# Kernel optimization log

Hardware: AMD Instinct MI355X
Metric: run time of the kernel (lower is better)

Reference implementation:

```python
import jax, jax.numpy as jnp
import numpy as np

D = 256; NH = 8; NL = 4; NP = 8; DFF = 1024; NQ = 300; BS = 8
DH = D // NH
_SHAPES = np.array([[100, 100], [50, 50], [25, 25], [13, 13]], dtype=np.int64)
S = int(_SHAPES.prod(1).sum())


def setup_inputs():
    key = jax.random.key(0)
    ks = jax.random.split(key, 24)
    rn = lambda k, sh, s=0.02: jax.random.normal(k, sh, jnp.float32) * s
    lsi = np.concatenate([[0], np.cumsum(_SHAPES.prod(1))[:-1]])
    return {
        'tgt': rn(ks[0], (NQ, BS, D), 1.0),
        'tgt_query_mask': rn(ks[1], (NQ, BS, D), 1.0),
        'tgt_reference_bboxs': jax.random.uniform(ks[2], (NQ, BS, 4), jnp.float32, 0.1, 0.5),
        'tgt_reference_masks': jax.random.uniform(ks[3], (NQ, BS, 32, 32), jnp.float32),
        'memory': rn(ks[4], (S, BS, D), 1.0),
        'in_proj_w': rn(ks[5], (3 * D, D)), 'in_proj_b': jnp.zeros((3 * D,), jnp.float32),
        'out_sa_w': rn(ks[6], (D, D)), 'out_sa_b': jnp.zeros((D,), jnp.float32),
        'norm2_g': jnp.ones((D,), jnp.float32), 'norm2_b': jnp.zeros((D,), jnp.float32),
        'value_w': rn(ks[7], (D, D)), 'value_b': jnp.zeros((D,), jnp.float32),
        'off_w': rn(ks[8], (NH * NL * NP * 2, D)), 'off_b': rn(ks[9], (NH * NL * NP * 2,), 0.5),
        'aw_w': rn(ks[10], (NH * NL * NP, D)), 'aw_b': jnp.zeros((NH * NL * NP,), jnp.float32),
        'out_ca_w': rn(ks[11], (D, D)), 'out_ca_b': jnp.zeros((D,), jnp.float32),
        'norm1_g': jnp.ones((D,), jnp.float32), 'norm1_b': jnp.zeros((D,), jnp.float32),
        'lin1_w': rn(ks[12], (DFF, D)), 'lin1_b': jnp.zeros((DFF,), jnp.float32),
        'lin2_w': rn(ks[13], (D, DFF)), 'lin2_b': jnp.zeros((D,), jnp.float32),
        'norm3_g': jnp.ones((D,), jnp.float32), 'norm3_b': jnp.zeros((D,), jnp.float32),
        'memory_key_padding_mask': jnp.zeros((BS, S), bool),
        'memory_spatial_shapes': jnp.asarray(_SHAPES, jnp.int32),
        'memory_level_start_index': jnp.asarray(lsi, jnp.int32),
    }


def _lin(x, w, b):
    return x @ w.T + b


def _ln(x, g, b):
    mu = x.mean(-1, keepdims=True)
    v = ((x - mu) ** 2).mean(-1, keepdims=True)
    return (x - mu) / jnp.sqrt(v + 1e-5) * g + b


def _ms_deform(query, ref, mem, pad_mask, spatial, lstart, vw, vb, ow, ob, aww, awb, outw, outb):
    # query/ref/mem: (bs, nq, D), (bs, nq, 4 cxcywh in [0,1]), (bs, S, D)
    bs, nq, _ = query.shape
    value = _lin(mem, vw, vb)
    value = jnp.where(pad_mask[:, :, None], 0.0, value).reshape(bs, -1, NH, DH)
    off = _lin(query, ow, ob).reshape(bs, nq, NH, NL, NP, 2)
    aw = jax.nn.softmax(_lin(query, aww, awb).reshape(bs, nq, NH, NL * NP), -1)
    aw = aw.reshape(bs, nq, NH, NL, NP)
    ref6 = ref[:, :, None, None, None, :]
    loc = ref6[..., :2] + off / NP * ref6[..., 2:4] * 0.5  # (bs,nq,NH,NL,NP,2)
    Hs = spatial[:, 0].reshape(1, 1, 1, NL, 1)
    Ws = spatial[:, 1].reshape(1, 1, 1, NL, 1)
    ls = lstart.reshape(1, 1, 1, NL, 1)
    Hf = Hs.astype(jnp.float32); Wf = Ws.astype(jnp.float32)
    # grid_sample align_corners=False pixel coords
    x = loc[..., 0] * Wf - 0.5
    y = loc[..., 1] * Hf - 0.5
    x0 = jnp.floor(x); y0 = jnp.floor(y)
    vT = value.transpose(2, 0, 1, 3)  # (NH,bs,S,DH)
    acc = jnp.zeros((bs, nq, NH, NL, NP, DH), jnp.float32)
    for dx in (0.0, 1.0):
        for dy in (0.0, 1.0):
            xi = x0 + dx; yi = y0 + dy
            w = (1.0 - jnp.abs(x - xi)) * (1.0 - jnp.abs(y - yi))
            valid = ((xi >= 0) & (xi < Wf) & (yi >= 0) & (yi < Hf)).astype(jnp.float32)
            xc = jnp.clip(xi, 0.0, Wf - 1.0).astype(jnp.int32)
            yc = jnp.clip(yi, 0.0, Hf - 1.0).astype(jnp.int32)
            idx = ls + yc * Ws + xc  # flat index into S, (bs,nq,NH,NL,NP)
            iT = idx.transpose(2, 0, 1, 3, 4).reshape(NH, bs, -1)
            g = jax.vmap(lambda v, i: jnp.take_along_axis(v, i[:, :, None], axis=1))(vT, iT)
            g = g.reshape(NH, bs, nq, NL, NP, DH).transpose(1, 2, 0, 3, 4, 5)
            acc = acc + (w * valid)[..., None] * g
    out = (acc * aw[..., None]).sum(axis=(3, 4)).reshape(bs, nq, D)
    return _lin(out, outw, outb)


def reference(tgt, tgt_query_mask, tgt_reference_bboxs, tgt_reference_masks, memory,
              in_proj_w, in_proj_b, out_sa_w, out_sa_b, norm2_g, norm2_b,
              value_w, value_b, off_w, off_b, aw_w, aw_b, out_ca_w, out_ca_b,
              norm1_g, norm1_b, lin1_w, lin1_b, lin2_w, lin2_b, norm3_g, norm3_b,
              memory_key_padding_mask, memory_spatial_shapes, memory_level_start_index):
    nq, bs, _ = tgt.shape
    # --- self attention (nn.MultiheadAttention, seq-first, eval mode) ---
    q = tgt + tgt_query_mask
    qh = _lin(q, in_proj_w[:D], in_proj_b[:D]).reshape(nq, bs, NH, DH)
    kh = _lin(q, in_proj_w[D:2 * D], in_proj_b[D:2 * D]).reshape(nq, bs, NH, DH)
    vh = _lin(tgt, in_proj_w[2 * D:], in_proj_b[2 * D:]).reshape(nq, bs, NH, DH)
    logits = jnp.einsum('qbhd,kbhd->bhqk', qh, kh) / np.sqrt(DH).astype(np.float32)
    attn = jax.nn.softmax(logits, -1)
    sa = jnp.einsum('bhqk,kbhd->qbhd', attn, vh).reshape(nq, bs, D)
    sa = _lin(sa, out_sa_w, out_sa_b)
    tgt = _ln(tgt + sa, norm2_g, norm2_b)
    # --- multi-scale deformable cross attention ---
    ca = _ms_deform((tgt + tgt_query_mask).transpose(1, 0, 2),
                    tgt_reference_bboxs.transpose(1, 0, 2),
                    memory.transpose(1, 0, 2),
                    memory_key_padding_mask, memory_spatial_shapes, memory_level_start_index,
                    value_w, value_b, off_w, off_b, aw_w, aw_b, out_ca_w, out_ca_b)
    tgt = _ln(tgt + ca.transpose(1, 0, 2), norm1_g, norm1_b)
    # --- FFN ---
    t2 = _lin(jax.nn.relu(_lin(tgt, lin1_w, lin1_b)), lin2_w, lin2_b)
    return _ln(tgt + t2, norm3_g, norm3_b)
```

## Files before the change

### kernel.cpp

```cpp
#include <hip/hip_runtime.h>
#include <hip/hip_bf16.h>
#include <math.h>

#define NQ 300
#define BSZ 8
#define DIM 256
#define NHEAD 8
#define ROWS 2400

typedef __attribute__((ext_vector_type(8))) short bf16x8;
typedef __attribute__((ext_vector_type(4))) float f32x4;

__device__ inline short f2bf(float f) {
  __hip_bfloat16 h = __float2bfloat16(f);
  return *reinterpret_cast<short*>(&h);
}
__device__ inline float bf2f(unsigned short u) {
  union { unsigned u; float f; } c;
  c.u = ((unsigned)u) << 16;
  return c.f;
}

#if __has_builtin(__builtin_amdgcn_global_load_lds)
__device__ inline void gld16(const void* gsrc, void* ldst, int lane) {
  (void)lane;
  auto g = (const __attribute__((address_space(1))) unsigned int*)gsrc;
  auto l = (__attribute__((address_space(3))) unsigned int*)ldst;
  __builtin_amdgcn_global_load_lds(g, l, 16, 0, 0);
}
#else
__device__ inline void gld16(const void* gsrc, void* ldst, int lane) {
  ((float4*)ldst)[lane] = *(const float4*)gsrc;
}
#endif

struct WEntry { const float* src; unsigned short* dst; int K; int gstart; };
struct WPack { WEntry e[8]; int total; };
__global__ __launch_bounds__(256) void wconv_kernel(WPack P) {
  int g = blockIdx.x * 256 + threadIdx.x;
  if (g >= P.total) return;
  int i = 0;
  while (i < 7 && g >= P.e[i + 1].gstart) ++i;
  const float* src = P.e[i].src;
  unsigned short* dst = P.e[i].dst;
  const int K = P.e[i].K;
  int gl = g - P.e[i].gstart;
  int gpr = K >> 3;
  int r = gl / gpr, gk = gl - r * gpr;
  int nb = r >> 6, rr = r & 63;
  int c = gk >> 3, g8 = gk & 7;
  const float* s = src + (size_t)r * K + gk * 8;
  float4 v0 = *(const float4*)s, v1 = *(const float4*)(s + 4);
  bf16x8 o;
  o[0] = f2bf(v0.x); o[1] = f2bf(v0.y); o[2] = f2bf(v0.z); o[3] = f2bf(v0.w);
  o[4] = f2bf(v1.x); o[5] = f2bf(v1.y); o[6] = f2bf(v1.z); o[7] = f2bf(v1.w);
  size_t byte = ((size_t)(nb * (K >> 6) + c) * 64 + rr) * 128 + ((g8 * 16) ^ ((rr & 7) << 4));
  *(bf16x8*)((char*)dst + byte) = o;
}

__global__ void bias_cat(const float* __restrict__ a, const float* __restrict__ b,
                         float* __restrict__ o) {
  int t = blockIdx.x * 256 + threadIdx.x;
  if (t < 512) o[t] = a[t];
  else if (t < 768) o[t] = b[t - 512];
}

template <bool VMASK>
__global__ __launch_bounds__(256) void vgemm(const float* __restrict__ A,
                                             const unsigned short* __restrict__ Wz,
                                             const float* __restrict__ bias,
                                             __hip_bfloat16* __restrict__ C, int M,
                                             const unsigned char* __restrict__ vmask,
                                             int Srows) {
  __shared__ char As[32768];
  __shared__ char Bsh[16384];
  const int tid = threadIdx.x, lane = tid & 63, wid = tid >> 6;
  const int wr = wid >> 1, wc = wid & 1;
  const int nb = blockIdx.x;
  const int m0 = blockIdx.y * 128;
  const int l15 = lane & 15, lk = lane >> 4;

  f32x4 acc[4][4];
#pragma unroll
  for (int i = 0; i < 4; ++i)
#pragma unroll
    for (int j = 0; j < 4; ++j) acc[i][j] = {0.f, 0.f, 0.f, 0.f};

  const float* asrc[8];
#pragma unroll
  for (int i = 0; i < 8; ++i) {
    int ach = wid * 8 + i;
    int rr = ach * 4 + lk;
    int gg = ((((l15 >> 1) ^ (rr & 7)) << 1) | (l15 & 1));
    int rrg = m0 + rr;
    if (rrg > M - 1) rrg = M - 1;
    asrc[i] = A + (size_t)rrg * 256 + gg * 4;
  }

  for (int c = 0; c < 4; ++c) {
    __syncthreads();
#pragma unroll
    for (int i = 0; i < 8; ++i) gld16(asrc[i] + c * 64, As + (wid * 8 + i) * 1024, lane);
#pragma unroll
    for (int i = 0; i < 4; ++i) {
      int bch = wid * 4 + i;
      const char* src = (const char*)Wz +
                        ((size_t)((2 * nb + (bch >> 3)) * 4 + c)) * 8192 +
                        (bch & 7) * 1024 + lane * 16;
      gld16(src, Bsh + bch * 1024, lane);
    }
    __syncthreads();
#pragma unroll
    for (int kk = 0; kk < 2; ++kk) {
      bf16x8 af[4], bfr[4];
#pragma unroll
      for (int i = 0; i < 4; ++i) {
        int rr = wr * 64 + i * 16 + l15;
        int g32 = kk * 4 + lk;
        int byte = rr * 256 + ((g32 * 32) ^ ((rr & 7) << 5));
        f32x4 lo = *(f32x4*)(As + byte);
        f32x4 hi = *(f32x4*)(As + byte + 16);
        bf16x8 o;
        o[0] = f2bf(lo[0]); o[1] = f2bf(lo[1]); o[2] = f2bf(lo[2]); o[3] = f2bf(lo[3]);
        o[4] = f2bf(hi[0]); o[5] = f2bf(hi[1]); o[6] = f2bf(hi[2]); o[7] = f2bf(hi[3]);
        af[i] = o;
      }
#pragma unroll
      for (int j = 0; j < 4; ++j) {
        int rr = wc * 64 + j * 16 + l15;
        int g = kk * 4 + lk;
        int byte = (rr >> 6) * 8192 + (rr & 63) * 128 + ((g * 16) ^ ((rr & 7) << 4));
        bfr[j] = *(bf16x8*)(Bsh + byte);
      }
#pragma unroll
      for (int i = 0; i < 4; ++i)
#pragma unroll
        for (int j = 0; j < 4; ++j)
          acc[i][j] = __builtin_amdgcn_mfma_f32_16x16x32_bf16(af[i], bfr[j], acc[i][j], 0, 0, 0);
    }
  }

#pragma unroll
  for (int i = 0; i < 4; ++i) {
#pragma unroll
    for (int r = 0; r < 4; ++r) {
      int row = m0 + wr * 64 + i * 16 + lk * 4 + r;
      if (row >= M) continue;
      float mfac = 1.f;
      if (VMASK) mfac = vmask[(size_t)(row & 7) * Srows + (row >> 3)] ? 0.f : 1.f;
#pragma unroll
      for (int j = 0; j < 4; ++j) {
        int col = nb * 128 + wc * 64 + j * 16 + l15;
        float v = acc[i][j][r] + bias[col];
        if (VMASK) v *= mfac;
        C[(size_t)row * 256 + col] = __float2bfloat16(v);
      }
    }
  }
}

template <int BM, bool RELU, bool ADDM, bool QKV>
__global__ __launch_bounds__(256) void sgemm(const float* __restrict__ A,
                                             const float* __restrict__ Am,
                                             const unsigned short* __restrict__ Wz,
                                             const float* __restrict__ bias,
                                             float* __restrict__ C0, float* __restrict__ C1,
                                             int M, int Ns, int K) {
  constexpr int WMT = BM / 2, AM = WMT / 16;
  __shared__ char As[BM * 128];
  __shared__ char Bsh[8192];
  const int tid = threadIdx.x, lane = tid & 63, wid = tid >> 6;
  const int wr = wid >> 1, wc = wid & 1;
  const int nb = blockIdx.x, m0 = blockIdx.y * BM;
  const int l15 = lane & 15, lk = lane >> 4;
  const bool useM = QKV ? (nb < 8) : ADDM;

  f32x4 acc[AM][2];
#pragma unroll
  for (int i = 0; i < AM; ++i)
#pragma unroll
    for (int j = 0; j < 2; ++j) acc[i][j] = {0.f, 0.f, 0.f, 0.f};

  const int nch = K >> 6;
  for (int c = 0; c < nch; ++c) {
    __syncthreads();
#pragma unroll
    for (int j = 0; j < BM / 32; ++j) {
      int gi = tid * (BM / 32) + j;
      int rr = gi >> 3, g = gi & 7;
      int rg = m0 + rr;
      float4 v0 = make_float4(0.f, 0.f, 0.f, 0.f), v1 = v0;
      if (rg < M) {
        const float* p = A + (size_t)rg * K + c * 64 + g * 8;
        v0 = *(const float4*)p;
        v1 = *(const float4*)(p + 4);
        if (useM) {
          const float* q = Am + (size_t)rg * K + c * 64 + g * 8;
          float4 w0 = *(const float4*)q, w1 = *(const float4*)(q + 4);
          v0.x += w0.x; v0.y += w0.y; v0.z += w0.z; v0.w += w0.w;
          v1.x += w1.x; v1.y += w1.y; v1.z += w1.z; v1.w += w1.w;
        }
      }
      bf16x8 o;
      o[0] = f2bf(v0.x); o[1] = f2bf(v0.y); o[2] = f2bf(v0.z); o[3] = f2bf(v0.w);
      o[4] = f2bf(v1.x); o[5] = f2bf(v1.y); o[6] = f2bf(v1.z); o[7] = f2bf(v1.w);
      int byte = rr * 128 + ((g * 16) ^ ((rr & 7) << 4));
      *(bf16x8*)(As + byte) = o;
    }
#pragma unroll
    for (int i = 0; i < 2; ++i) {
      const char* src = (const char*)Wz + ((size_t)(nb * nch + c)) * 8192 +
                        wid * 2048 + i * 1024 + lane * 16;
      gld16(src, Bsh + wid * 2048 + i * 1024, lane);
    }
    __syncthreads();
#pragma unroll
    for (int kk = 0; kk < 2; ++kk) {
      bf16x8 af[AM], bfr[2];
#pragma unroll
      for (int i = 0; i < AM; ++i) {
        int rr = wr * WMT + i * 16 + l15;
        int byte = rr * 128 + (((kk * 4 + lk) * 16) ^ ((rr & 7) << 4));
        af[i] = *(bf16x8*)(As + byte);
      }
#pragma unroll
      for (int j = 0; j < 2; ++j) {
        int rr = wc * 32 + j * 16 + l15;
        int byte = rr * 128 + (((kk * 4 + lk) * 16) ^ ((rr & 7) << 4));
        bfr[j] = *(bf16x8*)(Bsh + byte);
      }
#pragma unroll
      for (int i = 0; i < AM; ++i)
#pragma unroll
        for (int j = 0; j < 2; ++j)
          acc[i][j] = __builtin_amdgcn_mfma_f32_16x16x32_bf16(af[i], bfr[j], acc[i][j], 0, 0, 0);
    }
  }

  float* outp;
  int ostride, ocol0;
  if (QKV) {
    if (nb < 8) { outp = C0; ostride = 512; ocol0 = nb * 64; }
    else        { outp = C1; ostride = 256; ocol0 = (nb - 8) * 64; }
  } else {
    outp = C0; ostride = Ns; ocol0 = nb * 64;
  }
#pragma unroll
  for (int i = 0; i < AM; ++i) {
#pragma unroll
    for (int r = 0; r < 4; ++r) {
      int row = m0 + wr * WMT + i * 16 + lk * 4 + r;
      if (row >= M) continue;
#pragma unroll
      for (int j = 0; j < 2; ++j) {
        int cl = wc * 32 + j * 16 + l15;
        float v = acc[i][j][r] + bias[nb * 64 + cl];
        if (RELU) v = fmaxf(v, 0.f);
        outp[(size_t)row * ostride + ocol0 + cl] = v;
      }
    }
  }
}

__global__ __launch_bounds__(256) void attn_kernel(const float* __restrict__ cqk,
                                                   const float* __restrict__ cv,
                                                   float* __restrict__ out) {
  __shared__ float Ks[NQ][32];
  __shared__ float Vs[NQ][32];
  const int b = blockIdx.x, h = blockIdx.y, qt = blockIdx.z;
  const int tid = threadIdx.x;
  for (int i = tid; i < NQ * 8; i += 256) {
    int qi = i >> 3, c4 = (i & 7) * 4;
    *(float4*)&Ks[qi][c4] = *(const float4*)&cqk[((size_t)(qi * 8 + b)) * 512 + 256 + h * 32 + c4];
    *(float4*)&Vs[qi][c4] = *(const float4*)&cv[((size_t)(qi * 8 + b)) * 256 + h * 32 + c4];
  }
  __syncthreads();
  const int row = qt * 64 + (tid >> 2);
  const int qr = tid & 3;
  if (row >= NQ) return;
  float qv[8];
  const float* qptr = &cqk[((size_t)(row * 8 + b)) * 512 + h * 32 + qr * 8];
  *(float4*)&qv[0] = *(const float4*)&qptr[0];
  *(float4*)&qv[4] = *(const float4*)&qptr[4];
  const float scale = 0.17677669529663687f;
  float m = -3.0e38f, l = 0.f;
  float acc[8] = {0.f, 0.f, 0.f, 0.f, 0.f, 0.f, 0.f, 0.f};
  for (int k = 0; k < NQ; ++k) {
    const float* kr = &Ks[k][qr * 8];
    float p = 0.f;
#pragma unroll
    for (int j = 0; j < 8; ++j) p = fmaf(qv[j], kr[j], p);
    p += __shfl_xor(p, 1, 4);
    p += __shfl_xor(p, 2, 4);
    float s = p * scale;
    float mn = fmaxf(m, s);
    float corr = __expf(m - mn);
    float e = __expf(s - mn);
    l = l * corr + e;
    const float* vr = &Vs[k][qr * 8];
#pragma unroll
    for (int j = 0; j < 8; ++j) acc[j] = fmaf(acc[j], corr, e * vr[j]);
    m = mn;
  }
  float inv = 1.f / l;
  float* op = &out[((size_t)(row * 8 + b)) * 256 + h * 32 + qr * 8];
#pragma unroll
  for (int j = 0; j < 8; ++j) op[j] = acc[j] * inv;
}

__global__ __launch_bounds__(256) void resid_ln_kernel(const float* __restrict__ X,
                                                       const float* __restrict__ R,
                                                       const float* __restrict__ g,
                                                       const float* __restrict__ be,
                                                       float* __restrict__ out) {
  const int r = blockIdx.x, c = threadIdx.x;
  const size_t i = (size_t)r * 256 + c;
  float x = X[i] + R[i];
  float s = x;
#pragma unroll
  for (int o = 32; o; o >>= 1) s += __shfl_xor(s, o, 64);
  __shared__ float sm[4], sv[4];
  const int w = c >> 6;
  if ((c & 63) == 0) sm[w] = s;
  __syncthreads();
  float mu = (sm[0] + sm[1] + sm[2] + sm[3]) * (1.f / 256.f);
  float d = x - mu;
  float v = d * d;
#pragma unroll
  for (int o = 32; o; o >>= 1) v += __shfl_xor(v, o, 64);
  if ((c & 63) == 0) sv[w] = v;
  __syncthreads();
  float var = (sv[0] + sv[1] + sv[2] + sv[3]) * (1.f / 256.f);
  out[i] = d * (1.f / sqrtf(var + 1e-5f)) * g[c] + be[c];
}

__global__ __launch_bounds__(256) void deform_kernel(const unsigned short* __restrict__ value,
                                                     const float* __restrict__ offaw,
                                                     const float* __restrict__ bbox,
                                                     const int* __restrict__ spatial,
                                                     const int* __restrict__ lstart,
                                                     float* __restrict__ out, int S) {
  __shared__ int sH[4], sW[4], sL[4];
  __shared__ float sbb[4];
  const int r = blockIdx.x;
  const int b = r & 7;
  const int tid = threadIdx.x;
  if (tid < 4) {
    sH[tid] = spatial[tid * 2];
    sW[tid] = spatial[tid * 2 + 1];
    sL[tid] = lstart[tid];
    sbb[tid] = bbox[(size_t)r * 4 + tid];
  }
  __syncthreads();
  const float cx = sbb[0], cy = sbb[1], bw = sbb[2], bh = sbb[3];
  float ox = offaw[(size_t)r * 768 + (size_t)tid * 2];
  float oy = offaw[(size_t)r * 768 + (size_t)tid * 2 + 1];
  float a = offaw[(size_t)r * 768 + 512 + tid];
  float mx = a;
#pragma unroll
  for (int o = 16; o; o >>= 1) mx = fmaxf(mx, __shfl_xor(mx, o, 32));
  float e = __expf(a - mx);
  float ssum = e;
#pragma unroll
  for (int o = 16; o; o >>= 1) ssum += __shfl_xor(ssum, o, 32);
  float myaw = e / ssum;

  float acc = 0.f;
  const size_t vb = (size_t)b * 256 + (size_t)tid;
  for (int lp = 0; lp < 32; ++lp) {
    const int l = lp >> 3;
    float bx = __shfl(ox, lp, 32);
    float by = __shfl(oy, lp, 32);
    float alp = __shfl(myaw, lp, 32);
    const float Wf = (float)sW[l], Hf = (float)sH[l];
    const int ls = sL[l], Wi = sW[l];
    float lx = cx + bx * 0.0625f * bw;
    float ly = cy + by * 0.0625f * bh;
    float x = lx * Wf - 0.5f;
    float y = ly * Hf - 0.5f;
    float x0 = floorf(x), y0 = floorf(y);
    float fx = x - x0, fy = y - y0;
    float tap = 0.f;
#pragma unroll
    for (int t = 0; t < 4; ++t) {
      float xi = x0 + (float)(t & 1);
      float yi = y0 + (float)(t >> 1);
      if (xi >= 0.f && yi >= 0.f && xi < Wf && yi < Hf) {
        float wx = (t & 1) ? fx : (1.f - fx);
        float wy = (t >> 1) ? fy : (1.f - fy);
        int idx = ls + (int)yi * Wi + (int)xi;
        tap = fmaf(wx * wy, bf2f(value[(size_t)idx * 2048 + vb]), tap);
      }
    }
    acc = fmaf(alp, tap, acc);
  }
  out[(size_t)r * 256 + tid] = acc;
}

extern "C" void kernel_launch(void* const* d_in, const int* in_sizes, int n_in, void* d_out,
                              int out_size, void* d_ws, size_t ws_size, hipStream_t stream) {
  (void)n_in; (void)out_size; (void)ws_size;
  const float* tgt = (const float*)d_in[0];
  const float* qmask = (const float*)d_in[1];
  const float* bbox = (const float*)d_in[2];
  const float* memory = (const float*)d_in[4];
  const float* ipw = (const float*)d_in[5];
  const float* ipb = (const float*)d_in[6];
  const float* osw = (const float*)d_in[7];
  const float* osb = (const float*)d_in[8];
  const float* n2g = (const float*)d_in[9];
  const float* n2b = (const float*)d_in[10];
  const float* vw = (const float*)d_in[11];
  const float* vbi = (const float*)d_in[12];
  const float* ow = (const float*)d_in[13];
  const float* ob = (const float*)d_in[14];
  const float* aww = (const float*)d_in[15];
  const float* awb = (const float*)d_in[16];
  const float* ocw = (const float*)d_in[17];
  const float* ocb = (const float*)d_in[18];
  const float* n1g = (const float*)d_in[19];
  const float* n1b = (const float*)d_in[20];
  const float* l1w = (const float*)d_in[21];
  const float* l1b = (const float*)d_in[22];
  const float* l2w = (const float*)d_in[23];
  const float* l2b = (const float*)d_in[24];
  const float* n3g = (const float*)d_in[25];
  const float* n3b = (const float*)d_in[26];
  const unsigned char* kpmask = (const unsigned char*)d_in[27];
  const int* spatial = (const int*)d_in[28];
  const int* lstart = (const int*)d_in[29];
  float* out = (float*)d_out;

  const int S = in_sizes[4] / (BSZ * DIM);
  const int Mv = S * BSZ;

  float* ws = (float*)d_ws;
  size_t o = 0;
  unsigned short* value = (unsigned short*)(ws + o); o += (size_t)Mv * DIM / 2;
  float* cqk = ws + o; o += (size_t)ROWS * 512;
  float* cv = ws + o; o += (size_t)ROWS * DIM;
  float* sraw = ws + o; o += (size_t)ROWS * DIM;
  float* proj = ws + o; o += (size_t)ROWS * DIM;
  float* tgt2 = ws + o; o += (size_t)ROWS * DIM;
  float* tgt3 = ws + o; o += (size_t)ROWS * DIM;
  float* ffn1 = ws + o; o += (size_t)ROWS * 1024;
  float* offaw = ws + o; o += (size_t)ROWS * 768;
  float* obaw = ws + o; o += 768;
  unsigned short* wz = (unsigned short*)(ws + o);
  unsigned short* ipw_z = wz;
  unsigned short* osw_z = ipw_z + 768 * 256;
  unsigned short* vw_z  = osw_z + 256 * 256;
  unsigned short* ow_z  = vw_z + 256 * 256;
  unsigned short* aww_z = ow_z + 512 * 256;
  unsigned short* ocw_z = aww_z + 256 * 256;
  unsigned short* l1w_z = ocw_z + 256 * 256;
  unsigned short* l2w_z = l1w_z + 1024 * 256;

  WPack P;
  int gs = 0;
  auto ent = [&](int idx, const float* s, unsigned short* d, int N_, int K_) {
    P.e[idx] = {s, d, K_, gs};
    gs += N_ * K_ / 8;
  };
  ent(0, ipw, ipw_z, 768, 256);
  ent(1, osw, osw_z, 256, 256);
  ent(2, vw, vw_z, 256, 256);
  ent(3, ow, ow_z, 512, 256);
  ent(4, aww, aww_z, 256, 256);
  ent(5, ocw, ocw_z, 256, 256);
  ent(6, l1w, l1w_z, 1024, 256);
  ent(7, l2w, l2w_z, 256, 1024);
  P.total = gs;
  wconv_kernel<<<dim3((gs + 255) / 256), 256, 0, stream>>>(P);
  bias_cat<<<dim3(3), 256, 0, stream>>>(ob, awb, obaw);

  sgemm<64, false, false, true><<<dim3(12, 38), 256, 0, stream>>>(
      tgt, qmask, ipw_z, ipb, cqk, cv, ROWS, 0, 256);
  attn_kernel<<<dim3(BSZ, NHEAD, (NQ + 63) / 64), 256, 0, stream>>>(cqk, cv, sraw);
  sgemm<32, false, false, false><<<dim3(4, 75), 256, 0, stream>>>(
      sraw, nullptr, osw_z, osb, proj, nullptr, ROWS, 256, 256);
  resid_ln_kernel<<<ROWS, 256, 0, stream>>>(proj, tgt, n2g, n2b, tgt2);
  vgemm<true><<<dim3(2, (Mv + 127) / 128), 256, 0, stream>>>(
      memory, vw_z, vbi, (__hip_bfloat16*)value, Mv, kpmask, S);
  sgemm<64, false, true, false><<<dim3(12, 38), 256, 0, stream>>>(
      tgt2, qmask, ow_z, obaw, offaw, nullptr, ROWS, 768, 256);
  deform_kernel<<<ROWS, 256, 0, stream>>>(value, offaw, bbox, spatial, lstart, sraw, S);
  sgemm<32, false, false, false><<<dim3(4, 75), 256, 0, stream>>>(
      sraw, nullptr, ocw_z, ocb, proj, nullptr, ROWS, 256, 256);
  resid_ln_kernel<<<ROWS, 256, 0, stream>>>(proj, tgt2, n1g, n1b, tgt3);
  sgemm<64, true, false, false><<<dim3(16, 38), 256, 0, stream>>>(
      tgt3, nullptr, l1w_z, l1b, ffn1, nullptr, ROWS, 1024, 256);
  sgemm<32, false, false, false><<<dim3(4, 75), 256, 0, stream>>>(
      ffn1, nullptr, l2w_z, l2b, proj, nullptr, ROWS, 256, 1024);
  resid_ln_kernel<<<ROWS, 256, 0, stream>>>(proj, tgt3, n3g, n3b, out);
}
```

Measured before the change: 425.8 us.

## Double-buffer LDS tiles in value and generic GEMMs with register prefetch

Both the value-projection GEMM and the generic GEMM now keep two LDS buffers for A and B. The next K-chunk is prefetched into registers and LDS while the current chunk is computed, which removes one barrier per iteration. The value GEMM also converts A from fp32 to bf16 once before it is written to LDS. Before, fp32 was stored in LDS and every warp converted it again on each fragment read, which halves the A tile footprint. The trade-off is higher register and LDS use, which may reduce occupancy.

```diff
diff --git a/kernel.cpp b/kernel.cpp
--- a/kernel.cpp
+++ b/kernel.cpp
@@ -33,6 +33,13 @@
   ((float4*)ldst)[lane] = *(const float4*)gsrc;
 }
 #endif
+
+__device__ inline bf16x8 cvt8(float4 v0, float4 v1) {
+  bf16x8 o;
+  o[0] = f2bf(v0.x); o[1] = f2bf(v0.y); o[2] = f2bf(v0.z); o[3] = f2bf(v0.w);
+  o[4] = f2bf(v1.x); o[5] = f2bf(v1.y); o[6] = f2bf(v1.z); o[7] = f2bf(v1.w);
+  return o;
+}
 
 struct WEntry { const float* src; unsigned short* dst; int K; int gstart; };
 struct WPack { WEntry e[8]; int total; };
@@ -51,11 +58,8 @@
   int c = gk >> 3, g8 = gk & 7;
   const float* s = src + (size_t)r * K + gk * 8;
   float4 v0 = *(const float4*)s, v1 = *(const float4*)(s + 4);
-  bf16x8 o;
-  o[0] = f2bf(v0.x); o[1] = f2bf(v0.y); o[2] = f2bf(v0.z); o[3] = f2bf(v0.w);
-  o[4] = f2bf(v1.x); o[5] = f2bf(v1.y); o[6] = f2bf(v1.z); o[7] = f2bf(v1.w);
   size_t byte = ((size_t)(nb * (K >> 6) + c) * 64 + rr) * 128 + ((g8 * 16) ^ ((rr & 7) << 4));
-  *(bf16x8*)((char*)dst + byte) = o;
+  *(bf16x8*)((char*)dst + byte) = cvt8(v0, v1);
 }
 
 __global__ void bias_cat(const float* __restrict__ a, const float* __restrict__ b,
@@ -72,8 +76,8 @@
                                              __hip_bfloat16* __restrict__ C, int M,
                                              const unsigned char* __restrict__ vmask,
                                              int Srows) {
-  __shared__ char As[32768];
-  __shared__ char Bsh[16384];
+  __shared__ char As[2][16384];
+  __shared__ char Bsh[2][16384];
   const int tid = threadIdx.x, lane = tid & 63, wid = tid >> 6;
   const int wr = wid >> 1, wc = wid & 1;
   const int nb = blockIdx.x;
@@ -86,57 +90,77 @@
 #pragma unroll
     for (int j = 0; j < 4; ++j) acc[i][j] = {0.f, 0.f, 0.f, 0.f};
 
-  const float* asrc[8];
-#pragma unroll
-  for (int i = 0; i < 8; ++i) {
-    int ach = wid * 8 + i;
-    int rr = ach * 4 + lk;
-    int gg = ((((l15 >> 1) ^ (rr & 7)) << 1) | (l15 & 1));
-    int rrg = m0 + rr;
-    if (rrg > M - 1) rrg = M - 1;
-    asrc[i] = A + (size_t)rrg * 256 + gg * 4;
-  }
-
+  const float* asrc[4];
+  int awby[4];
+#pragma unroll
+  for (int j = 0; j < 4; ++j) {
+    int gb = j * 256 + tid;
+    int row = gb >> 3, g8 = gb & 7;
+    int rg = m0 + row;
+    if (rg > M - 1) rg = M - 1;
+    asrc[j] = A + (size_t)rg * 256 + g8 * 8;
+    awby[j] = row * 128 + ((g8 * 16) ^ ((row & 7) << 4));
+  }
+
+  float4 ar[8];
+#define V_AISSUE(c)                                        \
+  {                                                        \
+    _Pragma("unroll") for (int j = 0; j < 4; ++j) {        \
+      const float* p = asrc[j] + (c) * 64;                 \
+      ar[2 * j] = *(const float4*)p;                       \
+      ar[2 * j + 1] = *(const float4*)(p + 4);             \
+    }                                                      \
+  }
+#define V_AWRITE(buf)                                      \
+  {                                                        \
+    _Pragma("unroll") for (int j = 0; j < 4; ++j)          \
+        *(bf16x8*)((buf) + awby[j]) = cvt8(ar[2 * j], ar[2 * j + 1]); \
+  }
+#define V_BGLD(c, buf)                                                          \
+  {                                                                             \
+    _Pragma("unroll") for (int i = 0; i < 4; ++i) {                             \
+      int bch = wid * 4 + i;                                                    \
+      const char* src = (const char*)Wz +                                       \
+                        ((size_t)((2 * nb + (bch >> 3)) * 4 + (c))) * 8192 +    \
+                        (bch & 7) * 1024 + lane * 16;                           \
+      gld16(src, (buf) + bch * 1024, lane);                                     \
+    }                                                                           \
+  }
+#define V_COMPUTE(Ab, Bb)                                                        \
+  {                                                                              \
+    _Pragma("unroll") for (int kk = 0; kk < 2; ++kk) {                           \
+      bf16x8 af[4], bfr[4];                                                      \
+      _Pragma("unroll") for (int i = 0; i < 4; ++i) {                            \
+        int rr = wr * 64 + i * 16 + l15;                                         \
+        af[i] = *(bf16x8*)((Ab) + rr * 128 + (((kk * 4 + lk) * 16) ^ ((rr & 7) << 4))); \
+      }                                                                          \
+      _Pragma("unroll") for (int j = 0; j < 4; ++j) {                            \
+        int rr = wc * 64 + j * 16 + l15;                                         \
+        bfr[j] = *(bf16x8*)((Bb) + (rr >> 6) * 8192 + (rr & 63) * 128 +          \
+                            (((kk * 4 + lk) * 16) ^ ((rr & 7) << 4)));           \
+      }                                                                          \
+      _Pragma("unroll") for (int i = 0; i < 4; ++i)                              \
+          _Pragma("unroll") for (int j = 0; j < 4; ++j)                          \
+              acc[i][j] = __builtin_amdgcn_mfma_f32_16x16x32_bf16(af[i], bfr[j], \
+                                                                  acc[i][j], 0, 0, 0); \
+    }                                                                            \
+  }
+
+  V_AISSUE(0);
+  V_BGLD(0, Bsh[0]);
+  V_AWRITE(As[0]);
+  __syncthreads();
+#pragma unroll
   for (int c = 0; c < 4; ++c) {
-    __syncthreads();
-#pragma unroll
-    for (int i = 0; i < 8; ++i) gld16(asrc[i] + c * 64, As + (wid * 8 + i) * 1024, lane);
-#pragma unroll
-    for (int i = 0; i < 4; ++i) {
-      int bch = wid * 4 + i;
-      const char* src = (const char*)Wz +
-                        ((size_t)((2 * nb + (bch >> 3)) * 4 + c)) * 8192 +
-                        (bch & 7) * 1024 + lane * 16;
-      gld16(src, Bsh + bch * 1024, lane);
-    }
-    __syncthreads();
-#pragma unroll
-    for (int kk = 0; kk < 2; ++kk) {
-      bf16x8 af[4], bfr[4];
-#pragma unroll
-      for (int i = 0; i < 4; ++i) {
-        int rr = wr * 64 + i * 16 + l15;
-        int g32 = kk * 4 + lk;
-        int byte = rr * 256 + ((g32 * 32) ^ ((rr & 7) << 5));
-        f32x4 lo = *(f32x4*)(As + byte);
-        f32x4 hi = *(f32x4*)(As + byte + 16);
-        bf16x8 o;
-        o[0] = f2bf(lo[0]); o[1] = f2bf(lo[1]); o[2] = f2bf(lo[2]); o[3] = f2bf(lo[3]);
-        o[4] = f2bf(hi[0]); o[5] = f2bf(hi[1]); o[6] = f2bf(hi[2]); o[7] = f2bf(hi[3]);
-        af[i] = o;
-      }
-#pragma unroll
-      for (int j = 0; j < 4; ++j) {
-        int rr = wc * 64 + j * 16 + l15;
-        int g = kk * 4 + lk;
-        int byte = (rr >> 6) * 8192 + (rr & 63) * 128 + ((g * 16) ^ ((rr & 7) << 4));
-        bfr[j] = *(bf16x8*)(Bsh + byte);
-      }
-#pragma unroll
-      for (int i = 0; i < 4; ++i)
-#pragma unroll
-        for (int j = 0; j < 4; ++j)
-          acc[i][j] = __builtin_amdgcn_mfma_f32_16x16x32_bf16(af[i], bfr[j], acc[i][j], 0, 0, 0);
+    const int cur = c & 1;
+    if (c < 3) {
+      V_AISSUE(c + 1);
+      V_BGLD(c + 1, Bsh[cur ^ 1]);
+    }
+    V_COMPUTE(As[cur], Bsh[cur]);
+    if (c < 3) {
+      V_AWRITE(As[cur ^ 1]);
+      __syncthreads();
     }
   }
 
@@ -166,9 +190,9 @@
                                              const float* __restrict__ bias,
                                              float* __restrict__ C0, float* __restrict__ C1,
                                              int M, int Ns, int K) {
-  constexpr int WMT = BM / 2, AM = WMT / 16;
-  __shared__ char As[BM * 128];
-  __shared__ char Bsh[8192];
+  constexpr int WMT = BM / 2, AM = WMT / 16, NA = BM / 32;
+  __shared__ char As[2][BM * 128];
+  __shared__ char Bsh[2][8192];
   const int tid = threadIdx.x, lane = tid & 63, wid = tid >> 6;
   const int wr = wid >> 1, wc = wid & 1;
   const int nb = blockIdx.x, m0 = blockIdx.y * BM;
@@ -182,58 +206,91 @@
     for (int j = 0; j < 2; ++j) acc[i][j] = {0.f, 0.f, 0.f, 0.f};
 
   const int nch = K >> 6;
+  const float* asrc[NA];
+  const float* amsrc[NA];
+  int awby[NA];
+  bool avalid[NA];
+#pragma unroll
+  for (int j = 0; j < NA; ++j) {
+    int gb = j * 256 + tid;
+    int row = gb >> 3, g8 = gb & 7;
+    int rg = m0 + row;
+    avalid[j] = rg < M;
+    if (rg > M - 1) rg = M - 1;
+    asrc[j] = A + (size_t)rg * K + g8 * 8;
+    amsrc[j] = (useM ? Am : A) + (size_t)rg * K + g8 * 8;
+    awby[j] = row * 128 + ((g8 * 16) ^ ((row & 7) << 4));
+  }
+
+  float4 ar[2 * NA], am2[2 * NA];
+#define S_AISSUE(c)                                          \
+  {                                                          \
+    _Pragma("unroll") for (int j = 0; j < NA; ++j) {         \
+      const float* p = asrc[j] + (c) * 64;                   \
+      ar[2 * j] = *(const float4*)p;                         \
+      ar[2 * j + 1] = *(const float4*)(p + 4);               \
+      if (useM) {                                            \
+        const float* q = amsrc[j] + (c) * 64;                \
+        am2[2 * j] = *(const float4*)q;                      \
+        am2[2 * j + 1] = *(const float4*)(q + 4);            \
+      }                                                      \
+    }                                                        \
+  }
+#define S_AWRITE(buf)                                                       \
+  {                                                                         \
+    _Pragma("unroll") for (int j = 0; j < NA; ++j) {                        \
+      float4 v0 = ar[2 * j], v1 = ar[2 * j + 1];                            \
+      if (useM) {                                                           \
+        float4 w0 = am2[2 * j], w1 = am2[2 * j + 1];                        \
+        v0.x += w0.x; v0.y += w0.y; v0.z += w0.z; v0.w += w0.w;             \
+        v1.x += w1.x; v1.y += w1.y; v1.z += w1.z; v1.w += w1.w;             \
+      }                                                                     \
+      if (!avalid[j]) { v0 = make_float4(0.f,0.f,0.f,0.f); v1 = v0; }       \
+      *(bf16x8*)((buf) + awby[j]) = cvt8(v0, v1);                           \
+    }                                                                       \
+  }
+#define S_BGLD(c, buf)                                                        \
+  {                                                                           \
+    _Pragma("unroll") for (int i = 0; i < 2; ++i) {                           \
+      int bch = wid * 2 + i;                                                  \
+      const char* src = (const char*)Wz + ((size_t)(nb * nch + (c))) * 8192 + \
+                        bch * 1024 + lane * 16;                               \
+      gld16(src, (buf) + bch * 1024, lane);                                   \
+    }                                                                         \
+  }
+#define S_COMPUTE(Ab, Bb)                                                        \
+  {                                                                              \
+    _Pragma("unroll") for (int kk = 0; kk < 2; ++kk) {                           \
+      bf16x8 af[AM], bfr[2];                                                     \
+      _Pragma("unroll") for (int i = 0; i < AM; ++i) {                           \
+        int rr = wr * WMT + i * 16 + l15;                                        \
+        af[i] = *(bf16x8*)((Ab) + rr * 128 + (((kk * 4 + lk) * 16) ^ ((rr & 7) << 4))); \
+      }                                                                          \
+      _Pragma("unroll") for (int j = 0; j < 2; ++j) {                            \
+        int rr = wc * 32 + j * 16 + l15;                                         \
+        bfr[j] = *(bf16x8*)((Bb) + rr * 128 + (((kk * 4 + lk) * 16) ^ ((rr & 7) << 4))); \
+      }                                                                          \
+      _Pragma("unroll") for (int i = 0; i < AM; ++i)                             \
+          _Pragma("unroll") for (int j = 0; j < 2; ++j)                          \
+              acc[i][j] = __builtin_amdgcn_mfma_f32_16x16x32_bf16(af[i], bfr[j], \
+                                                                  acc[i][j], 0, 0, 0); \
+    }                                                                            \
+  }
+
+  S_AISSUE(0);
+  S_BGLD(0, Bsh[0]);
+  S_AWRITE(As[0]);
+  __syncthreads();
   for (int c = 0; c < nch; ++c) {
-    __syncthreads();
-#pragma unroll
-    for (int j = 0; j < BM / 32; ++j) {
-      int gi = tid * (BM / 32) + j;
-      int rr = gi >> 3, g = gi & 7;
-      int rg = m0 + rr;
-      float4 v0 = make_float4(0.f, 0.f, 0.f, 0.f), v1 = v0;
-      if (rg < M) {
-        const float* p = A + (size_t)rg * K + c * 64 + g * 8;
-        v0 = *(const float4*)p;
-        v1 = *(const float4*)(p + 4);
-        if (useM) {
-          const float* q = Am + (size_t)rg * K + c * 64 + g * 8;
-          float4 w0 = *(const float4*)q, w1 = *(const float4*)(q + 4);
-          v0.x += w0.x; v0.y += w0.y; v0.z += w0.z; v0.w += w0.w;
-          v1.x += w1.x; v1.y += w1.y; v1.z += w1.z; v1.w += w1.w;
-        }
-      }
-      bf16x8 o;
-      o[0] = f2bf(v0.x); o[1] = f2bf(v0.y); o[2] = f2bf(v0.z); o[3] = f2bf(v0.w);
-      o[4] = f2bf(v1.x); o[5] = f2bf(v1.y); o[6] = f2bf(v1.z); o[7] = f2bf(v1.w);
-      int byte = rr * 128 + ((g * 16) ^ ((rr & 7) << 4));
-      *(bf16x8*)(As + byte) = o;
-    }
-#pragma unroll
-    for (int i = 0; i < 2; ++i) {
-      const char* src = (const char*)Wz + ((size_t)(nb * nch + c)) * 8192 +
-                        wid * 2048 + i * 1024 + lane * 16;
-      gld16(src, Bsh + wid * 2048 + i * 1024, lane);
-    }
-    __syncthreads();
-#pragma unroll
-    for (int kk = 0; kk < 2; ++kk) {
-      bf16x8 af[AM], bfr[2];
-#pragma unroll
-      for (int i = 0; i < AM; ++i) {
-        int rr = wr * WMT + i * 16 + l15;
-        int byte = rr * 128 + (((kk * 4 + lk) * 16) ^ ((rr & 7) << 4));
-        af[i] = *(bf16x8*)(As + byte);
-      }
-#pragma unroll
-      for (int j = 0; j < 2; ++j) {
-        int rr = wc * 32 + j * 16 + l15;
-        int byte = rr * 128 + (((kk * 4 + lk) * 16) ^ ((rr & 7) << 4));
-        bfr[j] = *(bf16x8*)(Bsh + byte);
-      }
-#pragma unroll
-      for (int i = 0; i < AM; ++i)
-#pragma unroll
-        for (int j = 0; j < 2; ++j)
-          acc[i][j] = __builtin_amdgcn_mfma_f32_16x16x32_bf16(af[i], bfr[j], acc[i][j], 0, 0, 0);
+    const int cur = c & 1;
+    if (c < nch - 1) {
+      S_AISSUE(c + 1);
+      S_BGLD(c + 1, Bsh[cur ^ 1]);
+    }
+    S_COMPUTE(As[cur], Bsh[cur]);
+    if (c < nch - 1) {
+      S_AWRITE(As[cur ^ 1]);
+      __syncthreads();
     }
   }
 
```

New measurement: 429.2 us. About the same (+0.8%).
